# Optimization experiments

Measured on AMD Instinct MI355X. Metric: run time of the kernel, lower is better.

The kernel has to match this reference:

```python
import jax, jax.numpy as jnp
import numpy as np

DIM = 1024
HEADS = 16
HEAD_DIM = DIM // HEADS
SCALE = DIM ** (-0.5)  # note: module scales by full dim, not head_dim


def setup_inputs() -> dict:
    key = jax.random.key(0)
    k1, k2, k3, k4 = jax.random.split(key, 4)
    B, N = 4, 2048
    x = jax.random.normal(k1, (B, N, DIM), dtype=jnp.float32)
    # nn.Linear(dim, 3*dim, bias=False): weight [3*dim, dim]
    w_qkv = jax.random.normal(k2, (3 * DIM, DIM), dtype=jnp.float32) * (DIM ** -0.5)
    # nn.Linear(dim, dim) with bias
    w_out = jax.random.normal(k3, (DIM, DIM), dtype=jnp.float32) * (DIM ** -0.5)
    b_out = jax.random.normal(k4, (DIM,), dtype=jnp.float32) * 0.01
    return {"x": x, "w_qkv": w_qkv, "w_out": w_out, "b_out": b_out}


def reference(x, w_qkv, w_out, b_out):
    b, n, _ = x.shape
    qkv = jnp.einsum('bnd,ed->bne', x, w_qkv)  # [b, n, 3*dim]
    # rearrange 'b n (qkv h d) -> qkv b h n d'
    qkv = qkv.reshape(b, n, 3, HEADS, HEAD_DIM)
    q, k, v = (qkv[:, :, i].transpose(0, 2, 1, 3) for i in range(3))  # [b, h, n, d]
    dots = jnp.einsum('bhid,bhjd->bhij', q, k) * SCALE
    attn = jax.nn.softmax(dots, axis=-1)
    out = jnp.einsum('bhij,bhjd->bhid', attn, v)
    out = out.transpose(0, 2, 1, 3).reshape(b, n, HEADS * HEAD_DIM)  # [b, n, dim]
    return jnp.einsum('bnd,ed->bne', out, w_out) + b_out
```

## Files before the change

kernel.cpp:

```cpp
#include <hip/hip_runtime.h>

typedef __bf16 bf16_t;
typedef __bf16 bf16x2 __attribute__((ext_vector_type(2)));
typedef __bf16 bf16x4 __attribute__((ext_vector_type(4)));
typedef __bf16 bf16x8 __attribute__((ext_vector_type(8)));
typedef float floatx4 __attribute__((ext_vector_type(4)));

__device__ __forceinline__ void gll16(const void* g, void* l) {
  __builtin_amdgcn_global_load_lds(
      (const __attribute__((address_space(1))) void*)g,
      (__attribute__((address_space(3))) void*)l, 16, 0, 0);
}

__device__ __forceinline__ bf16x8 cvt8(const float4 a, const float4 b) {
  bf16x8 v;
  v[0] = (bf16_t)a.x; v[1] = (bf16_t)a.y; v[2] = (bf16_t)a.z; v[3] = (bf16_t)a.w;
  v[4] = (bf16_t)b.x; v[5] = (bf16_t)b.y; v[6] = (bf16_t)b.z; v[7] = (bf16_t)b.w;
  return v;
}

__global__ __launch_bounds__(256)
void cvt_all(const float* __restrict__ x,  bf16_t* __restrict__ xb,
             const float* __restrict__ wq, bf16_t* __restrict__ wqb,
             const float* __restrict__ wo, bf16_t* __restrict__ wob)
{
  const int bid = blockIdx.x;
  const float* s;
  bf16_t* d;
  int i;
  if (bid < 4096)      { s = x;  d = xb;  i = bid * 256 + threadIdx.x; }
  else if (bid < 5632) { s = wq; d = wqb; i = (bid - 4096) * 256 + threadIdx.x; }
  else                 { s = wo; d = wob; i = (bid - 5632) * 256 + threadIdx.x; }
  const float4 a = ((const float4*)s)[2 * i];
  const float4 b = ((const float4*)s)[2 * i + 1];
  *(bf16x8*)(d + (size_t)i * 8) = cvt8(a, b);
}

template<bool C32>
__global__ __launch_bounds__(256, 3)
void gemm_bt(const bf16_t* __restrict__ Ab, const bf16_t* __restrict__ Wb,
             const float* __restrict__ bias, void* __restrict__ Cv,
             int M, int Nf, int K, int lda, int qcols, float qscale)
{
  __shared__ __align__(16) bf16_t lA[128 * 64];
  __shared__ __align__(16) bf16_t lB[128 * 64];

  const int tid  = threadIdx.x;
  const int wave = tid >> 6;
  const int lane = tid & 63;
  const int q    = lane >> 4;
  const int ln   = lane & 15;
  const int wm   = wave >> 1, wn = wave & 1;

  const int x     = blockIdx.x & 7;
  const int local = blockIdx.x >> 3;
  const int mt = x * 8 + (local & 7);
  const int nt = local >> 3;
  const int m0 = mt << 7, n0 = nt << 7;

  floatx4 acc[4][4] = {};

  for (int k0 = 0; k0 < K; k0 += 64) {
#pragma unroll
    for (int t = 0; t < 4; ++t) {
      const int rbase = t * 32 + wave * 8;
      const int r  = rbase + (lane >> 3);
      const int gc = (lane & 7) ^ (r & 7);
      gll16(Ab + (size_t)(m0 + r) * lda + k0 + gc * 8, lA + rbase * 64);
      gll16(Wb + (size_t)(n0 + r) * K   + k0 + gc * 8, lB + rbase * 64);
    }
    __syncthreads();

    bf16x8 af[4][2], bfr[4][2];
#pragma unroll
    for (int i = 0; i < 4; ++i) {
      const int r = wm * 64 + i * 16 + ln;
#pragma unroll
      for (int kt = 0; kt < 2; ++kt) {
        const int c = (kt * 4 + q) ^ (r & 7);
        af[i][kt] = *(const bf16x8*)(lA + r * 64 + c * 8);
      }
    }
#pragma unroll
    for (int j = 0; j < 4; ++j) {
      const int r = wn * 64 + j * 16 + ln;
#pragma unroll
      for (int kt = 0; kt < 2; ++kt) {
        const int c = (kt * 4 + q) ^ (r & 7);
        bfr[j][kt] = *(const bf16x8*)(lB + r * 64 + c * 8);
      }
    }
#pragma unroll
    for (int i = 0; i < 4; ++i)
#pragma unroll
      for (int j = 0; j < 4; ++j)
#pragma unroll
        for (int kt = 0; kt < 2; ++kt)
          acc[i][j] = __builtin_amdgcn_mfma_f32_16x16x32_bf16(af[i][kt], bfr[j][kt], acc[i][j], 0, 0, 0);
    __syncthreads();
  }

#pragma unroll
  for (int j = 0; j < 4; ++j) {
    const int col = n0 + wn * 64 + j * 16 + ln;
    const float bv = bias ? bias[col] : 0.0f;
    const float sc = (col < qcols) ? qscale : 1.0f;
#pragma unroll
    for (int i = 0; i < 4; ++i) {
      const int row = m0 + wm * 64 + i * 16 + q * 4;
#pragma unroll
      for (int r = 0; r < 4; ++r) {
        const float val = acc[i][j][r] * sc + bv;
        if constexpr (C32)
          ((float*)Cv)[(size_t)(row + r) * Nf + col] = val;
        else
          ((bf16_t*)Cv)[(size_t)(row + r) * Nf + col] = (bf16_t)val;
      }
    }
  }
}

__global__ __launch_bounds__(256, 2)
void attn_kernel(bf16_t* __restrict__ qkv)
{
  __shared__ __align__(16) bf16_t lK[2][128 * 64];
  __shared__ __align__(16) bf16_t lVT[64 * 128];
  __shared__ __align__(16) bf16_t lP[128 * 128];

  const int tid  = threadIdx.x;
  const int wave = tid >> 6;
  const int lane = tid & 63;
  const int q  = lane >> 4;
  const int ln = lane & 15;
  const int wm = wave >> 1, wn = wave & 1;

  const int hw = blockIdx.x;
  const int w  = (hw & 7) * 128 + (hw >> 3);
  const int qt = w & 15;
  const int h  = (w >> 4) & 15;
  const int b  = w >> 8;

  bf16_t* Qbase = qkv + (size_t)(b * 2048 + qt * 128) * 3072 + h * 64;
  const bf16_t* Kbase = qkv + (size_t)(b * 2048) * 3072 + 1024 + h * 64;
  const bf16_t* Vbase = qkv + (size_t)(b * 2048) * 3072 + 2048 + h * 64;

#pragma unroll
  for (int t = 0; t < 4; ++t) {
    const int rbase = t * 32 + wave * 8;
    const int r  = rbase + (lane >> 3);
    const int gc = (lane & 7) ^ (r & 7);
    gll16(Qbase + (size_t)r * 3072 + gc * 8, lP + rbase * 64);
    gll16(Kbase + (size_t)r * 3072 + gc * 8, lK[0] + rbase * 64);
  }
  __syncthreads();

  bf16x8 qf[4][2];
#pragma unroll
  for (int i = 0; i < 4; ++i) {
    const int r = wm * 64 + i * 16 + ln;
#pragma unroll
    for (int kt = 0; kt < 2; ++kt) {
      const int c = (kt * 4 + q) ^ (r & 7);
      qf[i][kt] = *(const bf16x8*)(lP + r * 64 + c * 8);
    }
  }

  bf16x8 vcur[2][2], vnxt[2][2];
#pragma unroll
  for (int it = 0; it < 2; ++it) {
    const bf16_t* src = Vbase + (size_t)(2 * lane) * 3072 + (wave + it * 4) * 8;
    vcur[it][0] = *(const bf16x8*)src;
    vcur[it][1] = *(const bf16x8*)(src + 3072);
  }

  floatx4 accO[2][4] = {};
  floatx4 accS[2] = {};

  bf16x8 ones;
#pragma unroll
  for (int j = 0; j < 8; ++j) ones[j] = (bf16_t)1.0f;

  for (int jt = 0; jt < 16; ++jt) {
    const bf16_t* lKc = lK[jt & 1];
    bf16_t*       lKn = lK[(jt & 1) ^ 1];

    __syncthreads();

#pragma unroll
    for (int it = 0; it < 2; ++it) {
      const int c = wave + it * 4;
#pragma unroll
      for (int j = 0; j < 8; ++j) {
        const int d  = c * 8 + j;
        const int ch = (lane >> 2) ^ (d & 7);
        bf16x2 pr;
        pr[0] = vcur[it][0][j];
        pr[1] = vcur[it][1][j];
        *(bf16x2*)(lVT + d * 128 + ch * 8 + ((2 * lane) & 7)) = pr;
      }
    }

    bf16x8 kf[4][2];
#pragma unroll
    for (int n = 0; n < 4; ++n) {
      const int r = wn * 64 + n * 16 + ln;
#pragma unroll
      for (int kt = 0; kt < 2; ++kt) {
        const int c = (kt * 4 + q) ^ (r & 7);
        kf[n][kt] = *(const bf16x8*)(lKc + r * 64 + c * 8);
      }
    }

    if (jt < 15) {
      const int j0n = (jt + 1) * 128;
#pragma unroll
      for (int t = 0; t < 4; ++t) {
        const int rbase = t * 32 + wave * 8;
        const int r  = rbase + (lane >> 3);
        const int gc = (lane & 7) ^ (r & 7);
        gll16(Kbase + (size_t)(j0n + r) * 3072 + gc * 8, lKn + rbase * 64);
      }
#pragma unroll
      for (int it = 0; it < 2; ++it) {
        const bf16_t* src = Vbase + (size_t)(j0n + 2 * lane) * 3072 + (wave + it * 4) * 8;
        vnxt[it][0] = *(const bf16x8*)src;
        vnxt[it][1] = *(const bf16x8*)(src + 3072);
      }
    }

    __builtin_amdgcn_s_setprio(1);
#pragma unroll
    for (int i = 0; i < 4; ++i) {
#pragma unroll
      for (int n = 0; n < 4; ++n) {
        floatx4 st = {0.0f, 0.0f, 0.0f, 0.0f};
        st = __builtin_amdgcn_mfma_f32_16x16x32_bf16(kf[i][0], qf[n][0], st, 0, 0, 0);
        st = __builtin_amdgcn_mfma_f32_16x16x32_bf16(kf[i][1], qf[n][1], st, 0, 0, 0);
        bf16x4 pk;
#pragma unroll
        for (int r = 0; r < 4; ++r)
          pk[r] = (bf16_t)__builtin_amdgcn_exp2f(st[r]);
        const int m    = wm * 64 + n * 16 + ln;
        const int tok0 = wn * 64 + i * 16 + q * 4;
        *(bf16x4*)(lP + m * 128 + (((tok0 >> 3) ^ (m & 7)) << 3) + (tok0 & 7)) = pk;
      }
    }
    __builtin_amdgcn_s_setprio(0);

    __syncthreads();

    __builtin_amdgcn_s_setprio(1);
#pragma unroll
    for (int ks = 0; ks < 4; ++ks) {
      bf16x8 bv[4];
#pragma unroll
      for (int n = 0; n < 4; ++n) {
        const int d  = n * 16 + ln;
        const int cc = (ks * 4 + q) ^ (d & 7);
        bv[n] = *(const bf16x8*)(lVT + d * 128 + cc * 8);
      }
#pragma unroll
      for (int i = 0; i < 2; ++i) {
        const int m = wave * 32 + i * 16 + ln;
        const bf16x8 ap = *(const bf16x8*)(lP + m * 128 + (((ks * 4 + q) ^ (m & 7)) << 3));
#pragma unroll
        for (int n = 0; n < 4; ++n)
          accO[i][n] = __builtin_amdgcn_mfma_f32_16x16x32_bf16(ap, bv[n], accO[i][n], 0, 0, 0);
        accS[i] = __builtin_amdgcn_mfma_f32_16x16x32_bf16(ap, ones, accS[i], 0, 0, 0);
      }
    }
    __builtin_amdgcn_s_setprio(0);

    if (jt < 15) {
#pragma unroll
      for (int it = 0; it < 2; ++it) {
        vcur[it][0] = vnxt[it][0];
        vcur[it][1] = vnxt[it][1];
      }
    }
  }

#pragma unroll
  for (int i = 0; i < 2; ++i) {
#pragma unroll
    for (int r = 0; r < 4; ++r) {
      const int row = wave * 32 + i * 16 + q * 4 + r;
      const float rcp = 1.0f / fmaxf(accS[i][r], 1e-20f);
#pragma unroll
      for (int n = 0; n < 4; ++n) {
        const int col = n * 16 + ln;
        Qbase[(size_t)row * 3072 + col] = (bf16_t)(accO[i][n][r] * rcp);
      }
    }
  }
}

extern "C" void kernel_launch(void* const* d_in, const int* in_sizes, int n_in,
                              void* d_out, int out_size, void* d_ws, size_t ws_size,
                              hipStream_t stream)
{
  const float* x     = (const float*)d_in[0];
  const float* w_qkv = (const float*)d_in[1];
  const float* w_out = (const float*)d_in[2];
  const float* b_out = (const float*)d_in[3];
  float* out = (float*)d_out;

  bf16_t* qkv    = (bf16_t*)d_ws;
  bf16_t* xb     = qkv    + (size_t)8192 * 3072;
  bf16_t* wqkvb  = xb     + (size_t)8192 * 1024;
  bf16_t* woutb  = wqkvb  + (size_t)3072 * 1024;

  const float qs = 0.04508422f;

  cvt_all<<<dim3(6144), dim3(256), 0, stream>>>(x, xb, w_qkv, wqkvb, w_out, woutb);

  gemm_bt<false><<<dim3(64 * 24), dim3(256), 0, stream>>>(
      xb, wqkvb, nullptr, qkv, 8192, 3072, 1024, 1024, 1024, qs);
  attn_kernel<<<dim3(1024), dim3(256), 0, stream>>>(qkv);
  gemm_bt<true><<<dim3(64 * 8), dim3(256), 0, stream>>>(
      qkv, woutb, b_out, out, 8192, 1024, 1024, 3072, 0, 1.0f);
}
```

Before: 268.9 us.

## Double-buffer GEMM LDS tiles to overlap global loads with MFMA compute

```diff
diff --git a/kernel.cpp b/kernel.cpp
--- a/kernel.cpp
+++ b/kernel.cpp
@@ -10,6 +10,11 @@
   __builtin_amdgcn_global_load_lds(
       (const __attribute__((address_space(1))) void*)g,
       (__attribute__((address_space(3))) void*)l, 16, 0, 0);
+}
+
+__device__ __forceinline__ void drain_vmcnt() {
+  asm volatile("s_waitcnt vmcnt(0)" ::: "memory");
+  __builtin_amdgcn_sched_barrier(0);
 }
 
 __device__ __forceinline__ bf16x8 cvt8(const float4 a, const float4 b) {
@@ -37,13 +42,13 @@
 }
 
 template<bool C32>
-__global__ __launch_bounds__(256, 3)
+__global__ __launch_bounds__(256, 2)
 void gemm_bt(const bf16_t* __restrict__ Ab, const bf16_t* __restrict__ Wb,
              const float* __restrict__ bias, void* __restrict__ Cv,
              int M, int Nf, int K, int lda, int qcols, float qscale)
 {
-  __shared__ __align__(16) bf16_t lA[128 * 64];
-  __shared__ __align__(16) bf16_t lB[128 * 64];
+  __shared__ __align__(16) bf16_t lA[2][128 * 64];
+  __shared__ __align__(16) bf16_t lB[2][128 * 64];
 
   const int tid  = threadIdx.x;
   const int wave = tid >> 6;
@@ -58,18 +63,31 @@
   const int nt = local >> 3;
   const int m0 = mt << 7, n0 = nt << 7;
 
+  const int srb = (lane >> 3);
+  const int sgc = (lane & 7);
+
   floatx4 acc[4][4] = {};
 
-  for (int k0 = 0; k0 < K; k0 += 64) {
-#pragma unroll
-    for (int t = 0; t < 4; ++t) {
-      const int rbase = t * 32 + wave * 8;
-      const int r  = rbase + (lane >> 3);
-      const int gc = (lane & 7) ^ (r & 7);
-      gll16(Ab + (size_t)(m0 + r) * lda + k0 + gc * 8, lA + rbase * 64);
-      gll16(Wb + (size_t)(n0 + r) * K   + k0 + gc * 8, lB + rbase * 64);
-    }
-    __syncthreads();
+  const int kiters = K >> 6;
+
+  auto stage = [&](int buf, int k0s) {
+#pragma unroll
+    for (int tt = 0; tt < 4; ++tt) {
+      const int rbase = tt * 32 + wave * 8;
+      const int r  = rbase + srb;
+      const int gc = sgc ^ (r & 7);
+      gll16(Ab + (size_t)(m0 + r) * lda + k0s + gc * 8, lA[buf] + rbase * 64);
+      gll16(Wb + (size_t)(n0 + r) * K   + k0s + gc * 8, lB[buf] + rbase * 64);
+    }
+  };
+
+  stage(0, 0);
+  drain_vmcnt();
+  __syncthreads();
+
+  int cur = 0;
+  for (int t = 0; t < kiters; ++t) {
+    if (t + 1 < kiters) stage(cur ^ 1, (t + 1) << 6);
 
     bf16x8 af[4][2], bfr[4][2];
 #pragma unroll
@@ -78,7 +96,7 @@
 #pragma unroll
       for (int kt = 0; kt < 2; ++kt) {
         const int c = (kt * 4 + q) ^ (r & 7);
-        af[i][kt] = *(const bf16x8*)(lA + r * 64 + c * 8);
+        af[i][kt] = *(const bf16x8*)(lA[cur] + r * 64 + c * 8);
       }
     }
 #pragma unroll
@@ -87,9 +105,10 @@
 #pragma unroll
       for (int kt = 0; kt < 2; ++kt) {
         const int c = (kt * 4 + q) ^ (r & 7);
-        bfr[j][kt] = *(const bf16x8*)(lB + r * 64 + c * 8);
-      }
-    }
+        bfr[j][kt] = *(const bf16x8*)(lB[cur] + r * 64 + c * 8);
+      }
+    }
+    __builtin_amdgcn_s_setprio(1);
 #pragma unroll
     for (int i = 0; i < 4; ++i)
 #pragma unroll
@@ -97,7 +116,11 @@
 #pragma unroll
         for (int kt = 0; kt < 2; ++kt)
           acc[i][j] = __builtin_amdgcn_mfma_f32_16x16x32_bf16(af[i][kt], bfr[j][kt], acc[i][j], 0, 0, 0);
+    __builtin_amdgcn_s_setprio(0);
+
+    drain_vmcnt();
     __syncthreads();
+    cur ^= 1;
   }
 
 #pragma unroll
```

Result: faster. 262.5 us (-2.4%).

## Triple-buffer GEMM LDS tiles with async prefetch two K-steps ahead

Applied to the files above, without the earlier changes.

```diff
diff --git a/kernel.cpp b/kernel.cpp
--- a/kernel.cpp
+++ b/kernel.cpp
@@ -42,8 +42,8 @@
              const float* __restrict__ bias, void* __restrict__ Cv,
              int M, int Nf, int K, int lda, int qcols, float qscale)
 {
-  __shared__ __align__(16) bf16_t lA[128 * 64];
-  __shared__ __align__(16) bf16_t lB[128 * 64];
+  __shared__ __align__(16) bf16_t lA[3][128 * 32];
+  __shared__ __align__(16) bf16_t lB[3][128 * 32];
 
   const int tid  = threadIdx.x;
   const int wave = tid >> 6;
@@ -58,46 +58,56 @@
   const int nt = local >> 3;
   const int m0 = mt << 7, n0 = nt << 7;
 
+  const int kiters = K >> 5;
+
+  auto stage = [&](int buf, int k0s) {
+#pragma unroll
+    for (int tt = 0; tt < 2; ++tt) {
+      const int rbase = tt * 64 + wave * 16;
+      const int r  = rbase + (lane >> 2);
+      const int gc = (lane & 3) ^ ((r >> 1) & 3);
+      gll16(Ab + (size_t)(m0 + r) * lda + k0s + gc * 8, lA[buf] + rbase * 32);
+      gll16(Wb + (size_t)(n0 + r) * K   + k0s + gc * 8, lB[buf] + rbase * 32);
+    }
+  };
+
   floatx4 acc[4][4] = {};
 
-  for (int k0 = 0; k0 < K; k0 += 64) {
-#pragma unroll
-    for (int t = 0; t < 4; ++t) {
-      const int rbase = t * 32 + wave * 8;
-      const int r  = rbase + (lane >> 3);
-      const int gc = (lane & 7) ^ (r & 7);
-      gll16(Ab + (size_t)(m0 + r) * lda + k0 + gc * 8, lA + rbase * 64);
-      gll16(Wb + (size_t)(n0 + r) * K   + k0 + gc * 8, lB + rbase * 64);
-    }
-    __syncthreads();
-
-    bf16x8 af[4][2], bfr[4][2];
+  stage(0, 0);
+  stage(1, 32);
+
+  for (int t = 0; t < kiters; ++t) {
+    const int buf = t % 3;
+
+    if (t + 1 < kiters) {
+      asm volatile("s_waitcnt vmcnt(4)" ::: "memory");
+    } else {
+      asm volatile("s_waitcnt vmcnt(0)" ::: "memory");
+    }
+    __builtin_amdgcn_sched_barrier(0);
+    __builtin_amdgcn_s_barrier();
+    __builtin_amdgcn_sched_barrier(0);
+
+    bf16x8 af[4], bfr[4];
 #pragma unroll
     for (int i = 0; i < 4; ++i) {
       const int r = wm * 64 + i * 16 + ln;
-#pragma unroll
-      for (int kt = 0; kt < 2; ++kt) {
-        const int c = (kt * 4 + q) ^ (r & 7);
-        af[i][kt] = *(const bf16x8*)(lA + r * 64 + c * 8);
-      }
+      af[i] = *(const bf16x8*)(lA[buf] + r * 32 + (q ^ ((r >> 1) & 3)) * 8);
     }
 #pragma unroll
     for (int j = 0; j < 4; ++j) {
       const int r = wn * 64 + j * 16 + ln;
-#pragma unroll
-      for (int kt = 0; kt < 2; ++kt) {
-        const int c = (kt * 4 + q) ^ (r & 7);
-        bfr[j][kt] = *(const bf16x8*)(lB + r * 64 + c * 8);
-      }
-    }
+      bfr[j] = *(const bf16x8*)(lB[buf] + r * 32 + (q ^ ((r >> 1) & 3)) * 8);
+    }
+    __builtin_amdgcn_s_setprio(1);
 #pragma unroll
     for (int i = 0; i < 4; ++i)
 #pragma unroll
       for (int j = 0; j < 4; ++j)
-#pragma unroll
-        for (int kt = 0; kt < 2; ++kt)
-          acc[i][j] = __builtin_amdgcn_mfma_f32_16x16x32_bf16(af[i][kt], bfr[j][kt], acc[i][j], 0, 0, 0);
-    __syncthreads();
+        acc[i][j] = __builtin_amdgcn_mfma_f32_16x16x32_bf16(af[i], bfr[j], acc[i][j], 0, 0, 0);
+    __builtin_amdgcn_s_setprio(0);
+
+    if (t + 2 < kiters) stage((t + 2) % 3, (t + 2) << 5);
   }
 
 #pragma unroll
```

Result: faster. 262.6 us (-2.3%).
